# Kernel tuning notes

Measured on AMD Instinct MI355X. Metric: run time of the kernel, lower is better.

The kernel has to match this reference:

```python
import jax, jax.numpy as jnp
import numpy as np

N = 512        # input image side (== n after rounding, cor = n//2)
N_DET = 512
N_SPAN = 3
N_ANGLES_INIT = 1024
BATCH = 16
C = 1


def _splineB3(x2, r):
    sizex = len(x2)
    x2 = x2 - (x2[-1] + x2[0]) / 2
    stepx = x2[1] - x2[0]
    ri = int(np.ceil(2 * r))
    r = r * stepx
    c = int(np.ceil((sizex + 1) / 2.0))
    x2c = x2[c - 1]
    x = x2[c - ri - 1:c + ri]
    d = np.abs(x - x2c) / r
    B3 = np.zeros_like(x)
    for ix in range(-ri, ri + 1):
        i = ix + ri
        if d[i] < 1:
            B3[i] = (3 * d[i] ** 3 - 6 * d[i] ** 2 + 4) / 6
        elif d[i] < 2:
            B3[i] = (-d[i] ** 3 + 6 * d[i] ** 2 - 12 * d[i] + 8) / 6
    B3f = np.zeros_like(x2)
    B3f[c - ri - 1:c + ri] = B3
    return B3f


def _precompute():
    beta = np.pi / N_SPAN
    n = N  # ceil((512+0)/16)*16 == 512 since cor == n//2
    n_det = N_DET
    os_angles = int(max(round(3.0 * n / 2 / N_ANGLES_INIT), 1))  # == 1
    n_angles = os_angles * N_ANGLES_INIT
    angles = np.arange(n_angles) * np.pi / n_angles - beta / 2
    s = np.linspace(-1, 1, n_det)
    a_R = np.sin(beta / 2) / (1 + np.sin(beta / 2))
    a_m = (np.cos(beta / 2) - np.sin(beta / 2)) / (1 + np.sin(beta / 2))
    t = np.linspace(-np.pi / 2, np.pi / 2, 1000)
    w = a_R * np.cos(t) + (1 - a_R) + 1j * a_R * np.sin(t)
    g = np.nanmax(np.log(np.abs(w)) + np.log(np.cos(beta / 2 - np.arctan2(w.imag, w.real))))
    n_th = n_det
    n_rho = 2 * n_det
    d_th = 2 * beta / n_th
    d_rho = (g - np.log(a_m)) / n_rho
    th_lp = np.arange(-n_th / 2, n_th / 2) * d_th
    rho_lp = np.arange(-n_rho, 0) * d_rho
    b3_th = np.fft.fft(np.fft.ifftshift(_splineB3(th_lp, 1)))
    b3_rho = np.fft.fft(np.fft.ifftshift(_splineB3(rho_lp, 1)))
    b3_com = np.outer(b3_rho, b3_th)
    # ---- zeta coefficients (vectorized over k_rho) ----
    n_th_large = 4 * n_th
    k_rho = np.arange(-n_rho / 2, n_rho / 2, dtype='float32')
    th_sp_large = np.arange(-n_th_large / 2, n_th_large / 2) / n_th_large * beta * 2
    h = np.ones(n_th_large)
    correcting = 1 + np.array([-216254335, 679543284, -1412947389, 2415881496, -3103579086,
                               2939942400, -2023224114, 984515304, -321455811, 63253516,
                               -5675265]) / 958003200.0
    correcting[0] = 2 * (correcting[0] - 0.5)
    h[0] *= correcting[0]
    for j in range(1, len(correcting)):
        h[j] *= correcting[j]
        h[-j] *= correcting[j]
    expo = -2 * np.pi * 1j * k_rho / (g - np.log(a_m)) - 1
    fcosa = np.cos(th_sp_large)[None, :].astype('complex128') ** expo[:, None]
    fZ = np.fft.fftshift(np.fft.fft(np.fft.fftshift(h[None, :] * fcosa, axes=-1), axis=-1), axes=-1)
    fZ = fZ[:, n_th_large // 2 - n_th // 2: n_th_large // 2 + n_th // 2] * (th_sp_large[1] - th_sp_large[0])
    fZ[0] = 0
    fZ[:, 0] = 0
    zeta = np.fft.fftshift(fZ)
    const = np.sqrt(n_det * os_angles / n_angles) * np.pi / 4 / a_R / np.sqrt(2)
    zeta = zeta[:, :n_th // 2 + 1] * const
    zeta = zeta / b3_com[:, :n_th // 2 + 1]  # cubic interp prefilter compensation
    # ---- cartesian -> log-polar gather indices (floor, per span) ----
    tmp1 = np.outer(np.exp(rho_lp), np.cos(th_lp)).flatten()
    tmp2 = np.outer(np.exp(rho_lp), np.sin(th_lp)).flatten()
    idx_lp2c = []
    for k in range(N_SPAN):
        a = k * beta + beta / 2
        l1 = ((tmp1 - (1 - a_R)) * np.cos(a) - tmp2 * np.sin(a)) / a_R
        l2 = -(((tmp1 - (1 - a_R)) * np.sin(a) + tmp2 * np.cos(a)) / a_R)
        l1 = (l1 + 1) / 2 * (n_det - 1)
        l2 = (l2 + 1) / 2 * (n_det - 1)
        y = np.clip(np.floor(l1), 0, n_det - 2).astype(np.int32)
        x = np.clip(np.floor(l2), 0, n_det - 2).astype(np.int32)
        idx_lp2c.append(y * n_det + x)
    # ---- log-polar -> (angle, det) gather indices + span masks ----
    s0, th0 = np.meshgrid(s, angles)
    th0 = th0.flatten()
    s0 = s0.flatten()
    width_2 = n_angles * n_det // n_rho  # == n_th with these dims
    idx_p2lp = []
    pids = []
    with np.errstate(all='ignore'):
        for k in range(N_SPAN):
            pids.append(((th0 >= k * beta - beta / 2) & (th0 < k * beta + beta / 2)).astype(np.float32))
            th00 = th0 - k * beta
            p1 = (th00 - th_lp[0]) / (th_lp[-1] - th_lp[0]) * (n_th - 1)
            p2 = np.nan_to_num(np.log(s0 * a_R + (1 - a_R) * np.cos(th00)))
            p2 = (p2 - rho_lp[0]) / (rho_lp[-1] - rho_lp[0]) * (n_rho - 1)
            y = np.clip(np.floor(p2), 0, n_rho - 2).astype(np.int64)
            x = np.clip(np.floor(p1), 0, width_2 - 2).astype(np.int64)
            idx_p2lp.append((y * width_2 + x).astype(np.int32))
    return dict(
        n_rho=n_rho, n_th=n_th, n_angles=n_angles, n_det=n_det,
        zeta=jnp.asarray(zeta.astype(np.complex64)),
        e_rho=jnp.asarray(np.exp(rho_lp).astype(np.float32)).reshape(1, -1, 1, 1),
        idx_lp2c=jnp.asarray(np.stack(idx_lp2c)),
        idx_p2lp=jnp.asarray(np.stack(idx_p2lp)),
        pids=jnp.asarray(np.stack(pids)),
    )

_CONST = _precompute()


def setup_inputs() -> dict:
    key = jax.random.key(0)
    x = jax.random.normal(key, (BATCH, N, N, C), dtype=jnp.float32)
    return {"x": x}


def reference(x):
    c = _CONST
    b = x.shape[0]
    n_rho, n_th = c["n_rho"], c["n_th"]
    flat = x.reshape(b, N * N, C)
    out = jnp.zeros((b, c["n_angles"] * c["n_det"], C), dtype=x.dtype)
    for k in range(N_SPAN):
        # gather cartesian image onto log-polar grid (floor sampling)
        lp = flat[:, c["idx_lp2c"][k], :].reshape(b, n_rho, n_th, C) * c["e_rho"]
        # FFT-domain convolution with zeta kernel
        F = jnp.fft.rfft2(lp, axes=(1, 2)) * c["zeta"][None, :, :, None]
        gk = jnp.fft.irfft2(F, s=(n_rho, n_th), axes=(1, 2)).astype(x.dtype)
        # gather back onto (angle, detector) grid, masked by span membership
        samp = gk.reshape(b, n_rho * n_th, C)[:, c["idx_p2lp"][k], :]
        out = out + c["pids"][k][None, :, None] * samp
    return out.reshape(b, c["n_angles"], c["n_det"], C)
```

## Files before the change

### kernel.cpp

```cpp
#include <hip/hip_runtime.h>
#include <cmath>

#ifndef M_PI
#define M_PI 3.14159265358979323846
#endif

#define NIMG 512
#define NRHO 1024
#define NTH  512
#define ZROWS 256
#define GROWS 256
#define S4   520
#define PTOT (1024*512)
#define NSPAN 3
#define LPITEMS (NSPAN * NRHO * NTH)

struct Consts { double G_LA, d_rho, aR, dth, constv; };

static Consts compute_consts() {
  Consts c;
  const double beta = M_PI / 3.0;
  const double sb = sin(beta / 2.0), cb = cos(beta / 2.0);
  const double aR = sb / (1.0 + sb);
  const double am = (cb - sb) / (1.0 + sb);
  double g = -1e300;
  const double start = -M_PI / 2.0, stop = M_PI / 2.0;
  const double delta = (stop - start) / 999.0;
  for (int i = 0; i < 1000; ++i) {
    double t = (i == 999) ? stop : (double)i * delta + start;
    double wre = aR * cos(t) + (1.0 - aR);
    double wim = aR * sin(t);
    double v = log(hypot(wre, wim)) + log(cos(beta / 2.0 - atan2(wim, wre)));
    if (!std::isnan(v) && v > g) g = v;
  }
  c.aR    = aR;
  c.G_LA  = g - log(am);
  c.d_rho = c.G_LA / 1024.0;
  double t1 = (-1023.0 / 2048.0) * beta * 2.0;
  double t0 = (-1024.0 / 2048.0) * beta * 2.0;
  c.dth = t1 - t0;
  c.constv = sqrt(0.5) * M_PI / 4.0 / aR / sqrt(2.0);
  return c;
}
static const Consts g_C = compute_consts();

__device__ __forceinline__ float2 cmulf(float2 a, float2 b) {
  return make_float2(a.x * b.x - a.y * b.y, a.x * b.y + a.y * b.x);
}
__device__ __forceinline__ float2 cmulcf(float2 a, float2 w) {
  return make_float2(a.x * w.x + a.y * w.y, a.y * w.x - a.x * w.y);
}
__device__ __forceinline__ int SW(int i) { return i ^ ((i >> 5) & 31); }
__device__ __forceinline__ int PD(int i) { return i + (i >> 4); }
__device__ __forceinline__ int dr4_10(int v) {
  int r = 0;
  #pragma unroll
  for (int k = 0; k < 5; ++k) { r = (r << 2) | (v & 3); v >>= 2; }
  return r;
}
__device__ __forceinline__ void bf4f(float2 a, float2 b, float2 c, float2 d,
                                     float2& y0, float2& y1, float2& y2, float2& y3) {
  float2 A = make_float2(a.x + c.x, a.y + c.y);
  float2 C = make_float2(a.x - c.x, a.y - c.y);
  float2 B = make_float2(b.x + d.x, b.y + d.y);
  float2 D = make_float2(b.x - d.x, b.y - d.y);
  y0 = make_float2(A.x + B.x, A.y + B.y);
  y2 = make_float2(A.x - B.x, A.y - B.y);
  y1 = make_float2(C.x + D.y, C.y - D.x);
  y3 = make_float2(C.x - D.y, C.y + D.x);
}
__device__ __forceinline__ void bf4i(float2 u0, float2 u1, float2 u2, float2 u3,
                                     float2& z0, float2& z1, float2& z2, float2& z3) {
  float2 t0 = make_float2(u0.x + u2.x, u0.y + u2.y);
  float2 t1 = make_float2(u0.x - u2.x, u0.y - u2.y);
  float2 t2 = make_float2(u1.x + u3.x, u1.y + u3.y);
  float2 t3 = make_float2(u1.x - u3.x, u1.y - u3.y);
  z0 = make_float2(t0.x + t2.x, t0.y + t2.y);
  z2 = make_float2(t0.x - t2.x, t0.y - t2.y);
  z1 = make_float2(t1.x - t3.y, t1.y + t3.x);
  z3 = make_float2(t1.x + t3.y, t1.y - t3.x);
}
__device__ __forceinline__ double h_val(int jj) {
  const double ctab[11] = {-216254335.0, 679543284.0, -1412947389.0, 2415881496.0,
                           -3103579086.0, 2939942400.0, -2023224114.0, 984515304.0,
                           -321455811.0, 63253516.0, -5675265.0};
  int j = -1;
  if (jj <= 10) j = jj;
  else if (jj >= 2038) j = 2048 - jj;
  if (j < 0) return 1.0;
  double c = 1.0 + ctab[j] / 958003200.0;
  if (j == 0) c = 2.0 * (c - 0.5);
  return c;
}

__global__ __launch_bounds__(256) void k_pre(double* __restrict__ Ltab,
                                             double* __restrict__ amp,
                                             float2* __restrict__ tw1024f,
                                             float2* __restrict__ tw2048f,
                                             float* __restrict__ ertab,
                                             double d_rho) {
  int id = blockIdx.x * 256 + threadIdx.x;
  const double beta = M_PI / 3.0;
  if (id < 2048) {
    double th = ((double)(id - 1024) / 2048.0) * beta * 2.0;
    double L = log(cos(th));
    Ltab[id] = L;
    amp[id]  = h_val(id) * exp(-L);
  }
  if (id < 1024) {
    double a1 = -2.0 * M_PI * (double)id / 1024.0;
    double a2 = -2.0 * M_PI * (double)id / 2048.0;
    double s1, c1, s2, c2;
    sincos(a1, &s1, &c1); sincos(a2, &s2, &c2);
    tw1024f[id] = make_float2((float)c1, (float)s1);
    tw2048f[id] = make_float2((float)c2, (float)s2);
    ertab[id] = (float)exp((double)(id - 1024) * d_rho);
  }
}

__global__ __launch_bounds__(256) void k_zeta(const double* __restrict__ Ltab,
                                              const double* __restrict__ amp,
                                              const float2* __restrict__ tw2048f,
                                              float2* __restrict__ zetaT,
                                              double G_LA, double dth, double constv) {
  __shared__ float2 s[2048 + 128];
  __shared__ float2 twl[1024 + 64];
  const int i   = blockIdx.x;
  const int tid = threadIdx.x;
  for (int e = tid; e < 1024; e += 256) twl[PD(e)] = tw2048f[e];
  const double om = 2.0 * M_PI * (double)(i - 512) / G_LA;
  const double INV2PI = 1.0 / (2.0 * M_PI);
  for (int j = tid; j < 2048; j += 256) {
    int jj = (j + 1024) & 2047;
    double ph = -om * Ltab[jj] * INV2PI;
    ph -= floor(ph);
    float ang = (float)ph * 6.28318530717958647f;
    float sv, cv; __sincosf(ang, &sv, &cv);
    float a = (float)amp[jj];
    s[PD(__brev((unsigned)j) >> 21)] = make_float2(a * cv, a * sv);
  }
  for (int lh = 0; lh < 11; ++lh) {
    __syncthreads();
    for (int e = tid; e < 1024; e += 256) {
      int pos = e & ((1 << lh) - 1);
      int ia  = ((e >> lh) << (lh + 1)) | pos;
      float2 w = twl[PD(pos << (10 - lh))];
      float2 u = s[PD(ia)];
      float2 v = cmulf(s[PD(ia + (1 << lh))], w);
      s[PD(ia)]             = make_float2(u.x + v.x, u.y + v.y);
      s[PD(ia + (1 << lh))] = make_float2(u.x - v.x, u.y - v.y);
    }
  }
  __syncthreads();
  const int i2 = (i + 512) & 1023;
  const int p  = dr4_10(i2);
  const int pp = ((p & 15) << 6) | (p >> 4);
  const double b3r = (4.0 + 2.0 * cos(2.0 * M_PI * (double)i2 / 1024.0)) / 6.0;
  if (tid < 256) {
    int j2 = tid;
    float2 z = make_float2(0.f, 0.f);
    if (i != 0) {
      float2 F = s[PD(j2)];
      double b3t = (4.0 + 2.0 * cos(2.0 * M_PI * (double)j2 / 512.0)) / 6.0;
      double sc = dth * constv / (b3r * b3t) * (1.0 / (1024.0 * 512.0));
      z = make_float2((float)((double)F.x * sc), (float)((double)F.y * sc));
    }
    zetaT[(size_t)j2 * 1024 + pp] = z;
  }
}

__global__ __launch_bounds__(256) void k_idx_lp2c(int* __restrict__ idx1,
                                                  int* __restrict__ idx2,
                                                  double d_rho, double aR) {
  int q = blockIdx.x * 256 + threadIdx.x;
  const double beta = M_PI / 3.0;
  if (q < LPITEMS) {
    int span = q >> 19;
    int ql = q & (NRHO * NTH - 1);
    int i = ql >> 9, j = ql & 511;
    double d_th = 2.0 * beta / 512.0;
    double th = (double)(j - 256) * d_th;
    double er = exp((double)(i - 1024) * d_rho);
    double t1 = er * cos(th), t2 = er * sin(th);
    double a = (double)span * beta + beta / 2.0;
    double ca = cos(a), sa = sin(a);
    double l1 = ((t1 - (1.0 - aR)) * ca - t2 * sa) / aR;
    double l2 = -(((t1 - (1.0 - aR)) * sa + t2 * ca) / aR);
    l1 = (l1 + 1.0) / 2.0 * 511.0;
    l2 = (l2 + 1.0) / 2.0 * 511.0;
    double fy = floor(l1); fy = fy < 0.0 ? 0.0 : (fy > 510.0 ? 510.0 : fy);
    double fx = floor(l2); fx = fx < 0.0 ? 0.0 : (fx > 510.0 ? 510.0 : fx);
    idx1[q] = (int)fy * 512 + (int)fx;
  } else {
    int p = q - LPITEMS;
    const int t = p >> 9;
    const int d = p & 511;
    const int span = (3 * t) >> 10;
    double th0 = (double)t * M_PI / 1024.0 - beta / 2.0;
    double th00 = th0 - (double)span * beta;
    double d_th = 2.0 * beta / 512.0;
    double th_lp0 = -256.0 * d_th, th_lpL = 255.0 * d_th;
    double p1 = (th00 - th_lp0) / (th_lpL - th_lp0) * 511.0;
    double s0v = (d == 511) ? 1.0 : (double)d * (2.0 / 511.0) - 1.0;
    double p2 = log(s0v * aR + (1.0 - aR) * cos(th00));
    double rho0 = -1024.0 * d_rho, rhoL = -1.0 * d_rho;
    p2 = (p2 - rho0) / (rhoL - rho0) * 1023.0;
    double fy = floor(p2); fy = fy < 0.0 ? 0.0 : (fy > 1022.0 ? 1022.0 : fy);
    double fx = floor(p1); fx = fx < 0.0 ? 0.0 : (fx > 510.0 ? 510.0 : fx);
    idx2[p] = (span << 18) | (((int)fx - 128) * 1024 + (int)fy);
  }
}

__global__ __launch_bounds__(256) void k_gather_rfft(const float* __restrict__ x,
                                                     const int* __restrict__ idx1,
                                                     const float2* __restrict__ tw1024f,
                                                     const float* __restrict__ ertab,
                                                     float2* __restrict__ T,
                                                     int b0) {
  __shared__ float2 s[4][S4];
  __shared__ float2 twl[256];
  const int bx   = blockIdx.x;
  const int g    = ((bx & 7) << 4) | (bx >> 3);
  const int i0   = g * 8;
  const int lb   = blockIdx.y;
  const int span = blockIdx.z;
  const int tid  = threadIdx.x;
  twl[tid] = tw1024f[2 * tid];
  const int w  = tid >> 6;
  const int l6 = tid & 63;
  const float er0 = ertab[i0 + 2 * w];
  const float er1 = ertab[i0 + 2 * w + 1];
  const float* xb = x + (size_t)(b0 + lb) * (NIMG * NIMG);
  const int4* ip0 = (const int4*)(idx1 + span * (NRHO * NTH) + (i0 + 2 * w) * 512);
  const int4* ip1 = ip0 + 128;
  int4 a0 = ip0[l6], a1 = ip0[l6 + 64];
  int4 c0 = ip1[l6], c1 = ip1[l6 + 64];
  float v0[8], v1[8];
  v0[0] = xb[a0.x]; v0[1] = xb[a0.y]; v0[2] = xb[a0.z]; v0[3] = xb[a0.w];
  v0[4] = xb[a1.x]; v0[5] = xb[a1.y]; v0[6] = xb[a1.z]; v0[7] = xb[a1.w];
  v1[0] = xb[c0.x]; v1[1] = xb[c0.y]; v1[2] = xb[c0.z]; v1[3] = xb[c0.w];
  v1[4] = xb[c1.x]; v1[5] = xb[c1.y]; v1[6] = xb[c1.z]; v1[7] = xb[c1.w];
  float* sm = (float*)s[w];
  #pragma unroll
  for (int u = 0; u < 8; ++u) {
    int j = 4 * l6 + ((u & 4) << 6) + (u & 3);
    int slot = __brev((unsigned)j) >> 23;
    sm[2 * SW(slot) + 0] = v0[u] * er0;
    sm[2 * SW(slot) + 1] = v1[u] * er1;
  }
  #pragma unroll
  for (int lh = 0; lh < 8; lh += 2) {
    __syncthreads();
    const int q = 1 << lh;
    #pragma unroll
    for (int it = 0; it < 2; ++it) {
      int e = tid + (it << 8);
      int m = e >> 7, gq = e & 127;
      int pos = gq & (q - 1);
      int base = ((gq >> lh) << (lh + 2)) | pos;
      float2 w1 = twl[pos << (8 - lh)];
      float2 w2 = twl[pos << (7 - lh)];
      float2* smm = s[m];
      float2 a = smm[SW(base)];
      float2 b = smm[SW(base + q)];
      float2 c = smm[SW(base + 2 * q)];
      float2 d = smm[SW(base + 3 * q)];
      float2 wb = cmulf(b, w1), wd = cmulf(d, w1);
      float2 t0 = make_float2(a.x + wb.x, a.y + wb.y);
      float2 t1 = make_float2(a.x - wb.x, a.y - wb.y);
      float2 t2 = make_float2(c.x + wd.x, c.y + wd.y);
      float2 t3 = make_float2(c.x - wd.x, c.y - wd.y);
      float2 z2 = cmulf(t2, w2);
      float2 p3 = cmulf(t3, w2);
      float2 z3 = make_float2(p3.y, -p3.x);
      smm[SW(base)]         = make_float2(t0.x + z2.x, t0.y + z2.y);
      smm[SW(base + 2 * q)] = make_float2(t0.x - z2.x, t0.y - z2.y);
      smm[SW(base + q)]     = make_float2(t1.x + z3.x, t1.y + z3.y);
      smm[SW(base + 3 * q)] = make_float2(t1.x - z3.x, t1.y - z3.y);
    }
  }
  __syncthreads();
  #pragma unroll
  for (int it = 0; it < 4; ++it) {
    int e = tid + (it << 8);
    int m = e >> 8, b = e & 255;
    float2 w2 = twl[b];
    float2* smm = s[m];
    float2 u = smm[SW(b)];
    float2 vv = cmulf(smm[SW(b + 256)], w2);
    smm[SW(b)]       = make_float2(u.x + vv.x, u.y + vv.y);
    smm[SW(b + 256)] = make_float2(u.x - vv.x, u.y - vv.y);
  }
  __syncthreads();
  float2* Tb = T + (size_t)(span * gridDim.y + lb) * (ZROWS * NRHO);
  for (int it = 0; it < 8; ++it) {
    int e = tid + (it << 8);
    int k = e >> 3, rr = e & 7;
    int m = rr >> 1, pp = rr & 1;
    float2 Z  = s[m][SW(k)];
    float2 Zc = s[m][SW((512 - k) & 511)];
    float2 F;
    if (!pp) F = make_float2(0.5f * (Z.x + Zc.x), 0.5f * (Z.y - Zc.y));
    else     F = make_float2(0.5f * (Z.y + Zc.y), 0.5f * (Zc.x - Z.x));
    Tb[(size_t)k * NRHO + i0 + rr] = F;
  }
}

__global__ __launch_bounds__(256) void k_fft_rho(float2* __restrict__ T,
                                                 const float2* __restrict__ zetaT,
                                                 const float2* __restrict__ tw1024f) {
  __shared__ float2 s[4][1024 + 64];
  __shared__ float2 twl[1024 + 64];
  const int j0   = blockIdx.x * 4;
  const int lb   = blockIdx.y;
  const int span = blockIdx.z;
  const int tid  = threadIdx.x;
  const int bin  = tid >> 6;
  const int t6   = tid & 63;
  float2* rowb = T + ((size_t)(span * gridDim.y + lb) * ZROWS + j0 + bin) * NRHO;

  float2 r[4][4];
  #pragma unroll
  for (int c = 0; c < 4; ++c)
    #pragma unroll
    for (int a = 0; a < 4; ++a)
      r[c][a] = rowb[t6 + 64 * a + 256 * c];

  for (int e = tid; e < 1024; e += 256) twl[PD(e)] = tw1024f[e];
  __syncthreads();

  #pragma unroll
  for (int a = 0; a < 4; ++a) {
    int jj = t6 + 64 * a;
    float2 y0, y1, y2, y3;
    bf4f(r[0][a], r[1][a], r[2][a], r[3][a], y0, y1, y2, y3);
    r[0][a] = y0;
    r[1][a] = cmulf(y1, twl[PD(jj)]);
    r[2][a] = cmulf(y2, twl[PD(2 * jj)]);
    r[3][a] = cmulf(y3, twl[PD(3 * jj)]);
  }
  {
    float2 w1 = twl[PD(4 * t6)], w2 = twl[PD(8 * t6)], w3 = twl[PD(12 * t6)];
    #pragma unroll
    for (int c = 0; c < 4; ++c) {
      float2 y0, y1, y2, y3;
      bf4f(r[c][0], r[c][1], r[c][2], r[c][3], y0, y1, y2, y3);
      r[c][0] = y0; r[c][1] = cmulf(y1, w1); r[c][2] = cmulf(y2, w2); r[c][3] = cmulf(y3, w3);
    }
  }
  #pragma unroll
  for (int c = 0; c < 4; ++c)
    #pragma unroll
    for (int a = 0; a < 4; ++a)
      s[bin][PD(t6 + 64 * a + 256 * c)] = r[c][a];
  __syncthreads();

  const int B64 = t6 >> 2, b2 = t6 & 3;
  const int fbase = 64 * B64 + b2;
  #pragma unroll
  for (int c = 0; c < 4; ++c)
    #pragma unroll
    for (int a = 0; a < 4; ++a)
      r[c][a] = s[bin][PD(fbase + 4 * a + 16 * c)];
  #pragma unroll
  for (int a = 0; a < 4; ++a) {
    int ji = 16 * (b2 + 4 * a);
    float2 y0, y1, y2, y3;
    bf4f(r[0][a], r[1][a], r[2][a], r[3][a], y0, y1, y2, y3);
    r[0][a] = y0;
    r[1][a] = cmulf(y1, twl[PD(ji)]);
    r[2][a] = cmulf(y2, twl[PD(2 * ji)]);
    r[3][a] = cmulf(y3, twl[PD(3 * ji)]);
  }
  {
    float2 w1 = twl[PD(64 * b2)], w2 = twl[PD(128 * b2)], w3 = twl[PD(192 * b2)];
    #pragma unroll
    for (int c = 0; c < 4; ++c) {
      float2 y0, y1, y2, y3;
      bf4f(r[c][0], r[c][1], r[c][2], r[c][3], y0, y1, y2, y3);
      r[c][0] = y0; r[c][1] = cmulf(y1, w1); r[c][2] = cmulf(y2, w2); r[c][3] = cmulf(y3, w3);
    }
  }
  #pragma unroll
  for (int c = 0; c < 4; ++c)
    #pragma unroll
    for (int a = 0; a < 4; ++a)
      s[bin][PD(fbase + 4 * a + 16 * c)] = r[c][a];
  __syncthreads();

  {
    const float2* zp = zetaT + (size_t)(j0 + bin) * NRHO;
    #pragma unroll
    for (int u = 0; u < 4; ++u) {
      int o0 = 16 * t6 + 4 * u;
      float2 a0 = s[bin][PD(o0)],     a1 = s[bin][PD(o0 + 1)];
      float2 a2 = s[bin][PD(o0 + 2)], a3 = s[bin][PD(o0 + 3)];
      float2 y0, y1, y2, y3;
      bf4f(a0, a1, a2, a3, y0, y1, y2, y3);
      float2 q0 = zp[64 * (4 * u + 0) + t6];
      float2 q1 = zp[64 * (4 * u + 1) + t6];
      float2 q2 = zp[64 * (4 * u + 2) + t6];
      float2 q3 = zp[64 * (4 * u + 3) + t6];
      y0 = cmulf(y0, q0); y1 = cmulf(y1, q1); y2 = cmulf(y2, q2); y3 = cmulf(y3, q3);
      float2 z0, z1, z2, z3;
      bf4i(y0, y1, y2, y3, z0, z1, z2, z3);
      s[bin][PD(o0)]     = z0; s[bin][PD(o0 + 1)] = z1;
      s[bin][PD(o0 + 2)] = z2; s[bin][PD(o0 + 3)] = z3;
    }
  }
  __syncthreads();

  #pragma unroll
  for (int c = 0; c < 4; ++c)
    #pragma unroll
    for (int a = 0; a < 4; ++a)
      r[c][a] = s[bin][PD(fbase + 4 * a + 16 * c)];
  {
    float2 w1 = twl[PD(64 * b2)], w2 = twl[PD(128 * b2)], w3 = twl[PD(192 * b2)];
    #pragma unroll
    for (int c = 0; c < 4; ++c) {
      float2 u1 = cmulcf(r[c][1], w1);
      float2 u2 = cmulcf(r[c][2], w2);
      float2 u3 = cmulcf(r[c][3], w3);
      bf4i(r[c][0], u1, u2, u3, r[c][0], r[c][1], r[c][2], r[c][3]);
    }
  }
  #pragma unroll
  for (int a = 0; a < 4; ++a) {
    int ji = 16 * (b2 + 4 * a);
    float2 u1 = cmulcf(r[1][a], twl[PD(ji)]);
    float2 u2 = cmulcf(r[2][a], twl[PD(2 * ji)]);
    float2 u3 = cmulcf(r[3][a], twl[PD(3 * ji)]);
    bf4i(r[0][a], u1, u2, u3, r[0][a], r[1][a], r[2][a], r[3][a]);
  }
  #pragma unroll
  for (int c = 0; c < 4; ++c)
    #pragma unroll
    for (int a = 0; a < 4; ++a)
      s[bin][PD(fbase + 4 * a + 16 * c)] = r[c][a];
  __syncthreads();

  #pragma unroll
  for (int c = 0; c < 4; ++c)
    #pragma unroll
    for (int a = 0; a < 4; ++a)
      r[c][a] = s[bin][PD(t6 + 64 * a + 256 * c)];
  {
    float2 w1 = twl[PD(4 * t6)], w2 = twl[PD(8 * t6)], w3 = twl[PD(12 * t6)];
    #pragma unroll
    for (int c = 0; c < 4; ++c) {
      float2 u1 = cmulcf(r[c][1], w1);
      float2 u2 = cmulcf(r[c][2], w2);
      float2 u3 = cmulcf(r[c][3], w3);
      bf4i(r[c][0], u1, u2, u3, r[c][0], r[c][1], r[c][2], r[c][3]);
    }
  }
  #pragma unroll
  for (int a = 0; a < 4; ++a) {
    int jj = t6 + 64 * a;
    float2 u1 = cmulcf(r[1][a], twl[PD(jj)]);
    float2 u2 = cmulcf(r[2][a], twl[PD(2 * jj)]);
    float2 u3 = cmulcf(r[3][a], twl[PD(3 * jj)]);
    bf4i(r[0][a], u1, u2, u3, r[0][a], r[1][a], r[2][a], r[3][a]);
  }
  #pragma unroll
  for (int c = 0; c < 4; ++c)
    #pragma unroll
    for (int a = 0; a < 4; ++a)
      rowb[t6 + 64 * a + 256 * c] = r[c][a];
}

__global__ __launch_bounds__(256) void k_irfft_th(const float2* __restrict__ T,
                                                  const float2* __restrict__ tw1024f,
                                                  float* __restrict__ gkT) {
  __shared__ float2 s[4][S4];
  __shared__ float2 twl[256];
  const int i0   = blockIdx.x * 8;
  const int lb   = blockIdx.y;
  const int span = blockIdx.z;
  const int tid  = threadIdx.x;
  twl[tid] = tw1024f[2 * tid];
  const float2* Tb = T + (size_t)(span * gridDim.y + lb) * (ZROWS * NRHO);
  __syncthreads();
  for (int it = 0; it < 8; ++it) {
    int e = tid + (it << 8);
    int k = e >> 3, rr = e & 7;
    int m = rr >> 1, p = rr & 1;
    s[m][SW(k + 256 * p)] = Tb[(size_t)k * NRHO + i0 + rr];
  }
  __syncthreads();
  float2 Zr[8];
  for (int it = 0; it < 8; ++it) {
    int e = tid + (it << 8);
    int m = e >> 9, k = e & 511;
    float2 z;
    if (k == 256) z = make_float2(0.f, 0.f);
    else {
      int k2 = (k < 256) ? k : 512 - k;
      float2 F0 = s[m][SW(k2)];
      float2 F1 = s[m][SW(256 + k2)];
      if (k2 == 0) { F0.y = 0.f; F1.y = 0.f; }
      if (k < 256) z = make_float2(F0.x - F1.y, F0.y + F1.x);
      else         z = make_float2(F0.x + F1.y, F1.x - F0.y);
    }
    Zr[it] = z;
  }
  __syncthreads();
  for (int it = 0; it < 8; ++it) {
    int e = tid + (it << 8);
    int m = e >> 9, k = e & 511;
    s[m][SW(k)] = Zr[it];
  }
  #pragma unroll
  for (int lh = 8; lh >= 2; lh -= 2) {
    __syncthreads();
    const int h = 1 << (lh - 1);
    #pragma unroll
    for (int it = 0; it < 2; ++it) {
      int e = tid + (it << 8);
      int m = e >> 7, gq = e & 127;
      int pos = gq & (h - 1);
      int base = ((gq >> (lh - 1)) << (lh + 1)) | pos;
      float2 wa = twl[pos << (8 - lh)];
      float2 w2 = twl[pos << (9 - lh)];
      float2* sm = s[m];
      float2 a = sm[SW(base)];
      float2 b = sm[SW(base + h)];
      float2 c = sm[SW(base + 2 * h)];
      float2 d = sm[SW(base + 3 * h)];
      float2 ap = make_float2(a.x + c.x, a.y + c.y);
      float2 cp = cmulcf(make_float2(a.x - c.x, a.y - c.y), wa);
      float2 bp = make_float2(b.x + d.x, b.y + d.y);
      float2 tt = cmulcf(make_float2(b.x - d.x, b.y - d.y), wa);
      float2 dp = make_float2(-tt.y, tt.x);
      sm[SW(base)]         = make_float2(ap.x + bp.x, ap.y + bp.y);
      sm[SW(base + h)]     = cmulcf(make_float2(ap.x - bp.x, ap.y - bp.y), w2);
      sm[SW(base + 2 * h)] = make_float2(cp.x + dp.x, cp.y + dp.y);
      sm[SW(base + 3 * h)] = cmulcf(make_float2(cp.x - dp.x, cp.y - dp.y), w2);
    }
  }
  __syncthreads();
  #pragma unroll
  for (int it = 0; it < 4; ++it) {
    int e = tid + (it << 8);
    int m = e >> 8, b = e & 255;
    int ia = b << 1;
    float2* sm = s[m];
    float2 u = sm[SW(ia)];
    float2 v = sm[SW(ia + 1)];
    sm[SW(ia)]     = make_float2(u.x + v.x, u.y + v.y);
    sm[SW(ia + 1)] = make_float2(u.x - v.x, u.y - v.y);
  }
  __syncthreads();
  float* gb = gkT + (size_t)(span * gridDim.y + lb) * (GROWS * NRHO);
  for (int it = 0; it < 8; ++it) {
    int e = tid + (it << 8);
    int ro = e >> 3, rr = e & 7;
    int j = ro + 128;
    int jslot = __brev((unsigned)j) >> 23;
    float2 z = s[rr >> 1][SW(jslot)];
    gb[(size_t)ro * NRHO + i0 + rr] = (rr & 1) ? z.y : z.x;
  }
}

__global__ __launch_bounds__(256) void k_scatter(const float* __restrict__ gkT,
                                                 const int* __restrict__ idx2,
                                                 float* __restrict__ out,
                                                 int b0, int chunk) {
  int p = blockIdx.x * 256 + threadIdx.x;
  if (p >= PTOT) return;
  int v = idx2[p];
  int span = v >> 18;
  int idx  = v & 0x3FFFF;
  const float* gsp = gkT + (size_t)span * chunk * (GROWS * NRHO) + idx;
  for (int lb = 0; lb < chunk; ++lb)
    out[(size_t)(b0 + lb) * PTOT + p] = gsp[(size_t)lb * (GROWS * NRHO)];
}

extern "C" void kernel_launch(void* const* d_in, const int* in_sizes, int n_in,
                              void* d_out, int out_size, void* d_ws, size_t ws_size,
                              hipStream_t stream) {
  (void)n_in; (void)out_size;
  const float* x = (const float*)d_in[0];
  float* out = (float*)d_out;
  const int batch = in_sizes[0] / (NIMG * NIMG);

  const size_t zeta_b = (size_t)ZROWS * NRHO * sizeof(float2);
  const size_t idx_b  = (size_t)NSPAN * NRHO * NTH * sizeof(int);
  const size_t idx2_b = (size_t)PTOT * sizeof(int);
  const size_t tab_b  = 2048 * sizeof(double) * 2 + 1024 * sizeof(float2) * 2
                      + 1024 * sizeof(float);
  const size_t per_b  = (size_t)NSPAN * ((size_t)ZROWS * NRHO * sizeof(float2)
                      + (size_t)GROWS * NRHO * sizeof(float));
  int chunk = batch;
  while (chunk > 1 && zeta_b + idx_b + idx2_b + tab_b + (size_t)chunk * per_b > ws_size)
    chunk >>= 1;

  char* ws = (char*)d_ws;
  float2* zetaT   = (float2*)ws;  ws += zeta_b;
  int*    idx1    = (int*)ws;     ws += idx_b;
  int*    idx2    = (int*)ws;     ws += idx2_b;
  double* Ltab    = (double*)ws;  ws += 2048 * sizeof(double);
  double* amp     = (double*)ws;  ws += 2048 * sizeof(double);
  float2* tw1024f = (float2*)ws;  ws += 1024 * sizeof(float2);
  float2* tw2048f = (float2*)ws;  ws += 1024 * sizeof(float2);
  float*  ertab   = (float*)ws;   ws += 1024 * sizeof(float);
  float2* T       = (float2*)ws;  ws += (size_t)NSPAN * chunk * ZROWS * NRHO * sizeof(float2);
  float*  gkT     = (float*)ws;

  k_pre     <<<dim3(8),    dim3(256), 0, stream>>>(Ltab, amp, tw1024f, tw2048f,
                                                   ertab, g_C.d_rho);
  k_zeta    <<<dim3(1024), dim3(256), 0, stream>>>(Ltab, amp, tw2048f, zetaT,
                                                   g_C.G_LA, g_C.dth, g_C.constv);
  k_idx_lp2c<<<dim3((LPITEMS + PTOT) / 256), dim3(256), 0, stream>>>(idx1, idx2,
                                                                     g_C.d_rho, g_C.aR);

  for (int b0 = 0; b0 < batch; b0 += chunk) {
    int c = (b0 + chunk <= batch) ? chunk : (batch - b0);
    k_gather_rfft<<<dim3(NRHO / 8, c, NSPAN), dim3(256), 0, stream>>>(x, idx1, tw1024f,
                                                                      ertab, T, b0);
    k_fft_rho    <<<dim3(ZROWS / 4, c, NSPAN), dim3(256), 0, stream>>>(T, zetaT, tw1024f);
    k_irfft_th   <<<dim3(NRHO / 8, c, NSPAN), dim3(256), 0, stream>>>(T, tw1024f, gkT);
    k_scatter    <<<dim3(PTOT / 256), dim3(256), 0, stream>>>(gkT, idx2, out, b0, c);
  }
}
```

Measured before the change: 283.5 us.

## Compute scatter indices inline and permute lp2c index layout for strided gather

The idx2 index table is no longer precomputed and stored. k_scatter now computes each output's log-polar source index on the fly in double precision, which removes the idx2 write and read traffic at the cost of extra math per output point. The idx1 table is also stored in a permuted order, and the matching j mapping in k_gather_rfft changes, so each thread's int4 loads cover columns strided by 128 instead of consecutive ones. This changes the access pattern of the image gather.

Result: faster. 274.3 us (-3.3%).

```diff
diff --git a/kernel.cpp b/kernel.cpp
--- a/kernel.cpp
+++ b/kernel.cpp
@@ -13,7 +13,6 @@
 #define S4   520
 #define PTOT (1024*512)
 #define NSPAN 3
-#define LPITEMS (NSPAN * NRHO * NTH)
 
 struct Consts { double G_LA, d_rho, aR, dth, constv; };
 
@@ -170,45 +169,25 @@
 }
 
 __global__ __launch_bounds__(256) void k_idx_lp2c(int* __restrict__ idx1,
-                                                  int* __restrict__ idx2,
                                                   double d_rho, double aR) {
   int q = blockIdx.x * 256 + threadIdx.x;
+  int span = q >> 19;
+  int ql = q & (NRHO * NTH - 1);
+  int i = ql >> 9, j = ql & 511;
   const double beta = M_PI / 3.0;
-  if (q < LPITEMS) {
-    int span = q >> 19;
-    int ql = q & (NRHO * NTH - 1);
-    int i = ql >> 9, j = ql & 511;
-    double d_th = 2.0 * beta / 512.0;
-    double th = (double)(j - 256) * d_th;
-    double er = exp((double)(i - 1024) * d_rho);
-    double t1 = er * cos(th), t2 = er * sin(th);
-    double a = (double)span * beta + beta / 2.0;
-    double ca = cos(a), sa = sin(a);
-    double l1 = ((t1 - (1.0 - aR)) * ca - t2 * sa) / aR;
-    double l2 = -(((t1 - (1.0 - aR)) * sa + t2 * ca) / aR);
-    l1 = (l1 + 1.0) / 2.0 * 511.0;
-    l2 = (l2 + 1.0) / 2.0 * 511.0;
-    double fy = floor(l1); fy = fy < 0.0 ? 0.0 : (fy > 510.0 ? 510.0 : fy);
-    double fx = floor(l2); fx = fx < 0.0 ? 0.0 : (fx > 510.0 ? 510.0 : fx);
-    idx1[q] = (int)fy * 512 + (int)fx;
-  } else {
-    int p = q - LPITEMS;
-    const int t = p >> 9;
-    const int d = p & 511;
-    const int span = (3 * t) >> 10;
-    double th0 = (double)t * M_PI / 1024.0 - beta / 2.0;
-    double th00 = th0 - (double)span * beta;
-    double d_th = 2.0 * beta / 512.0;
-    double th_lp0 = -256.0 * d_th, th_lpL = 255.0 * d_th;
-    double p1 = (th00 - th_lp0) / (th_lpL - th_lp0) * 511.0;
-    double s0v = (d == 511) ? 1.0 : (double)d * (2.0 / 511.0) - 1.0;
-    double p2 = log(s0v * aR + (1.0 - aR) * cos(th00));
-    double rho0 = -1024.0 * d_rho, rhoL = -1.0 * d_rho;
-    p2 = (p2 - rho0) / (rhoL - rho0) * 1023.0;
-    double fy = floor(p2); fy = fy < 0.0 ? 0.0 : (fy > 1022.0 ? 1022.0 : fy);
-    double fx = floor(p1); fx = fx < 0.0 ? 0.0 : (fx > 510.0 ? 510.0 : fx);
-    idx2[p] = (span << 18) | (((int)fx - 128) * 1024 + (int)fy);
-  }
+  double d_th = 2.0 * beta / 512.0;
+  double th = (double)(j - 256) * d_th;
+  double er = exp((double)(i - 1024) * d_rho);
+  double t1 = er * cos(th), t2 = er * sin(th);
+  double a = (double)span * beta + beta / 2.0;
+  double ca = cos(a), sa = sin(a);
+  double l1 = ((t1 - (1.0 - aR)) * ca - t2 * sa) / aR;
+  double l2 = -(((t1 - (1.0 - aR)) * sa + t2 * ca) / aR);
+  l1 = (l1 + 1.0) / 2.0 * 511.0;
+  l2 = (l2 + 1.0) / 2.0 * 511.0;
+  double fy = floor(l1); fy = fy < 0.0 ? 0.0 : (fy > 510.0 ? 510.0 : fy);
+  double fx = floor(l2); fx = fx < 0.0 ? 0.0 : (fx > 510.0 ? 510.0 : fx);
+  idx1[span * (NRHO * NTH) + i * 512 + 4 * (j & 127) + (j >> 7)] = (int)fy * 512 + (int)fx;
 }
 
 __global__ __launch_bounds__(256) void k_gather_rfft(const float* __restrict__ x,
@@ -243,7 +222,7 @@
   float* sm = (float*)s[w];
   #pragma unroll
   for (int u = 0; u < 8; ++u) {
-    int j = 4 * l6 + ((u & 4) << 6) + (u & 3);
+    int j = 128 * (u & 3) + ((u & 4) << 4) + l6;
     int slot = __brev((unsigned)j) >> 23;
     sm[2 * SW(slot) + 0] = v0[u] * er0;
     sm[2 * SW(slot) + 1] = v1[u] * er1;
@@ -564,17 +543,30 @@
 }
 
 __global__ __launch_bounds__(256) void k_scatter(const float* __restrict__ gkT,
-                                                 const int* __restrict__ idx2,
                                                  float* __restrict__ out,
-                                                 int b0, int chunk) {
+                                                 int b0, int chunk,
+                                                 double d_rho, double aR) {
   int p = blockIdx.x * 256 + threadIdx.x;
   if (p >= PTOT) return;
-  int v = idx2[p];
-  int span = v >> 18;
-  int idx  = v & 0x3FFFF;
-  const float* gsp = gkT + (size_t)span * chunk * (GROWS * NRHO) + idx;
+  const int t = p >> 9;
+  const int d = p & 511;
+  const int span = (3 * t) >> 10;
+  const double beta = M_PI / 3.0;
+  double th0 = (double)t * M_PI / 1024.0 - beta / 2.0;
+  double th00 = th0 - (double)span * beta;
+  double d_th = 2.0 * beta / 512.0;
+  double th_lp0 = -256.0 * d_th, th_lpL = 255.0 * d_th;
+  double p1 = (th00 - th_lp0) / (th_lpL - th_lp0) * 511.0;
+  double s0v = (d == 511) ? 1.0 : (double)d * (2.0 / 511.0) - 1.0;
+  double p2 = log(s0v * aR + (1.0 - aR) * cos(th00));
+  double rho0 = -1024.0 * d_rho, rhoL = -1.0 * d_rho;
+  p2 = (p2 - rho0) / (rhoL - rho0) * 1023.0;
+  double fy = floor(p2); fy = fy < 0.0 ? 0.0 : (fy > 1022.0 ? 1022.0 : fy);
+  double fx = floor(p1); fx = fx < 0.0 ? 0.0 : (fx > 510.0 ? 510.0 : fx);
+  int idx = ((int)fx - 128) * 1024 + (int)fy;
+  const float* gsp = gkT + (size_t)span * chunk * (GROWS * NRHO);
   for (int lb = 0; lb < chunk; ++lb)
-    out[(size_t)(b0 + lb) * PTOT + p] = gsp[(size_t)lb * (GROWS * NRHO)];
+    out[(size_t)(b0 + lb) * PTOT + p] = gsp[(size_t)lb * (GROWS * NRHO) + idx];
 }
 
 extern "C" void kernel_launch(void* const* d_in, const int* in_sizes, int n_in,
@@ -587,19 +579,16 @@
 
   const size_t zeta_b = (size_t)ZROWS * NRHO * sizeof(float2);
   const size_t idx_b  = (size_t)NSPAN * NRHO * NTH * sizeof(int);
-  const size_t idx2_b = (size_t)PTOT * sizeof(int);
   const size_t tab_b  = 2048 * sizeof(double) * 2 + 1024 * sizeof(float2) * 2
                       + 1024 * sizeof(float);
   const size_t per_b  = (size_t)NSPAN * ((size_t)ZROWS * NRHO * sizeof(float2)
                       + (size_t)GROWS * NRHO * sizeof(float));
   int chunk = batch;
-  while (chunk > 1 && zeta_b + idx_b + idx2_b + tab_b + (size_t)chunk * per_b > ws_size)
-    chunk >>= 1;
+  while (chunk > 1 && zeta_b + idx_b + tab_b + (size_t)chunk * per_b > ws_size) chunk >>= 1;
 
   char* ws = (char*)d_ws;
   float2* zetaT   = (float2*)ws;  ws += zeta_b;
   int*    idx1    = (int*)ws;     ws += idx_b;
-  int*    idx2    = (int*)ws;     ws += idx2_b;
   double* Ltab    = (double*)ws;  ws += 2048 * sizeof(double);
   double* amp     = (double*)ws;  ws += 2048 * sizeof(double);
   float2* tw1024f = (float2*)ws;  ws += 1024 * sizeof(float2);
@@ -612,8 +601,7 @@
                                                    ertab, g_C.d_rho);
   k_zeta    <<<dim3(1024), dim3(256), 0, stream>>>(Ltab, amp, tw2048f, zetaT,
                                                    g_C.G_LA, g_C.dth, g_C.constv);
-  k_idx_lp2c<<<dim3((LPITEMS + PTOT) / 256), dim3(256), 0, stream>>>(idx1, idx2,
-                                                                     g_C.d_rho, g_C.aR);
+  k_idx_lp2c<<<dim3((NSPAN * NRHO * NTH) / 256), dim3(256), 0, stream>>>(idx1, g_C.d_rho, g_C.aR);
 
   for (int b0 = 0; b0 < batch; b0 += chunk) {
     int c = (b0 + chunk <= batch) ? chunk : (batch - b0);
@@ -621,6 +609,7 @@
                                                                       ertab, T, b0);
     k_fft_rho    <<<dim3(ZROWS / 4, c, NSPAN), dim3(256), 0, stream>>>(T, zetaT, tw1024f);
     k_irfft_th   <<<dim3(NRHO / 8, c, NSPAN), dim3(256), 0, stream>>>(T, tw1024f, gkT);
-    k_scatter    <<<dim3(PTOT / 256), dim3(256), 0, stream>>>(gkT, idx2, out, b0, c);
-  }
-}
+    k_scatter    <<<dim3(PTOT / 256), dim3(256), 0, stream>>>(gkT, out, b0, c,
+                                                              g_C.d_rho, g_C.aR);
+  }
+}
```
